# Kernel tuning notes

Measured on AMD Instinct MI355X. Metric: run time of the kernel, lower is better.

The kernel has to match this reference:

```python
import jax, jax.numpy as jnp
import numpy as np

N = 100000   # nodes
E = 800000   # edges
IN = 128     # input feature dim
H = 2        # heads
C = 64       # hidden_dim (per-head channels)
OUT = 40     # classes
L = 3        # num_layers
EPS = 1e-16  # matches torch_geometric.utils.softmax denominator eps


def setup_inputs() -> dict:
    key = jax.random.key(0)
    ks = jax.random.split(key, 4 * L + 6)
    inp = {}
    inp["x"] = jax.random.normal(ks[0], (N, IN), dtype=jnp.float32)
    inp["edge_index"] = jax.random.randint(ks[1], (2, E), 0, N, dtype=jnp.int32)
    dims = [IN] + [H * C] * (L - 1)
    ki = 2
    for l in range(L):
        d = dims[l]
        inp[f"W{l}"] = jax.random.normal(ks[ki], (H * C, d), dtype=jnp.float32) / np.float32(np.sqrt(d)); ki += 1
        inp[f"b{l}"] = jnp.zeros((H * C,), dtype=jnp.float32)
        inp[f"al{l}"] = jax.random.normal(ks[ki], (H, C), dtype=jnp.float32) * 0.1; ki += 1
        inp[f"ar{l}"] = jax.random.normal(ks[ki], (H, C), dtype=jnp.float32) * 0.1; ki += 1
    inp["Wp1"] = jax.random.normal(ks[ki], (C, H * C), dtype=jnp.float32) / np.float32(np.sqrt(H * C)); ki += 1
    inp["bp1"] = jnp.zeros((C,), dtype=jnp.float32)
    inp["Wp2"] = jax.random.normal(ks[ki], (OUT, C), dtype=jnp.float32) / np.float32(np.sqrt(C)); ki += 1
    inp["bp2"] = jnp.zeros((OUT,), dtype=jnp.float32)
    return inp


def _gat_layer(x, W, b, al, ar, src, dst):
    # lin_l == lin_r (shared weights in the original)
    h = (x @ W.T + b).reshape(-1, H, C)          # [N, H, C]
    alpha_l = al * h                              # source-side scores [N, H, C]
    alpha_r = ar * h                              # target-side scores [N, H, C]
    # per-edge raw attention logits; NOTE: original computes leaky_relu(alpha)
    # but then applies softmax to the RAW sum (faithful to source code).
    e = alpha_r[dst] + alpha_l[src]               # [E, H, C]
    m = jax.ops.segment_max(e, dst, num_segments=N)
    w = jnp.exp(e - m[dst])
    s = jax.ops.segment_sum(w, dst, num_segments=N)
    att = w / (s[dst] + EPS)                      # segment softmax per target node
    out = jax.ops.segment_sum(att * h[src], dst, num_segments=N)  # [N, H, C]
    return out.reshape(-1, H * C)


def reference(x, edge_index, W0, b0, al0, ar0, W1, b1, al1, ar1, W2, b2, al2, ar2,
              Wp1, bp1, Wp2, bp2):
    src, dst = edge_index[0], edge_index[1]
    layers = [(W0, b0, al0, ar0), (W1, b1, al1, ar1), (W2, b2, al2, ar2)]
    h = x
    for (W, b, al, ar) in layers:
        h = _gat_layer(h, W, b, al, ar, src, dst)
        h = jax.nn.relu(h)  # dropout p=0 -> identity
    h = h @ Wp1.T + bp1
    h = h @ Wp2.T + bp2
    return jax.nn.log_softmax(h, axis=1)
```

## Files before the change

kernel.cpp:

```cpp
#include <hip/hip_runtime.h>
#include <hip/hip_bf16.h>
#include <math.h>

#define NN 100000
#define EE 800000
#define DD 128
#define OUTC 40

typedef short bf16x8 __attribute__((ext_vector_type(8)));
typedef float f32x4 __attribute__((ext_vector_type(4)));

__device__ __forceinline__ ushort f2bf(float f) {
  unsigned u = __float_as_uint(f);
  u = (u + 0x7FFFu + ((u >> 16) & 1u)) >> 16;
  return (ushort)u;
}
__device__ __forceinline__ float bflo(unsigned u) { return __uint_as_float(u << 16); }
__device__ __forceinline__ float bfhi(unsigned u) { return __uint_as_float(u & 0xFFFF0000u); }

__device__ __forceinline__ int swz(int row, int kbyte) {
  return row * 256 + (kbyte ^ ((row & 7) << 4));
}

__global__ void k_hist(const int* __restrict__ dst, int* __restrict__ deg, int e) {
  int i = blockIdx.x * 256 + threadIdx.x;
  if (i < e) atomicAdd(&deg[dst[i]], 1);
}

__global__ __launch_bounds__(1024) void k_scan1(const int* __restrict__ deg, int* __restrict__ rp,
                                                int* __restrict__ bsum, int n) {
  __shared__ int s[1024];
  int t = threadIdx.x;
  int i = blockIdx.x * 1024 + t;
  s[t] = (i < n) ? deg[i] : 0;
  __syncthreads();
  for (int off = 1; off < 1024; off <<= 1) {
    int x = (t >= off) ? s[t - off] : 0;
    __syncthreads();
    s[t] += x;
    __syncthreads();
  }
  if (i < n) rp[i + 1] = s[t];
  if (t == 1023) bsum[blockIdx.x] = s[1023];
}

__global__ __launch_bounds__(128) void k_scan2(int* __restrict__ bsum, int nb) {
  __shared__ int s[128];
  int t = threadIdx.x;
  s[t] = (t < nb) ? bsum[t] : 0;
  __syncthreads();
  for (int off = 1; off < 128; off <<= 1) {
    int x = (t >= off) ? s[t - off] : 0;
    __syncthreads();
    s[t] += x;
    __syncthreads();
  }
  if (t < nb) bsum[t] = s[t];
}

__global__ void k_scan3(int* __restrict__ rp, const int* __restrict__ bsum,
                        int* __restrict__ cursor, int n) {
  int i = blockIdx.x * 256 + threadIdx.x;
  if (i == 0) { rp[0] = 0; cursor[0] = 0; }
  if (i < n) {
    int blk = i >> 10;
    int v = rp[i + 1] + ((blk > 0) ? bsum[blk - 1] : 0);
    rp[i + 1] = v;
    cursor[i + 1] = v;
  }
}

__global__ void k_scatter(const int* __restrict__ src, const int* __restrict__ dst,
                          int* __restrict__ cursor, int* __restrict__ col, int e) {
  int i = blockIdx.x * 256 + threadIdx.x;
  if (i < e) {
    int d = dst[i];
    int pos = atomicAdd(&cursor[d], 1);
    col[pos] = src[i];
  }
}

template<int NOUT, bool INF32, bool OUTBF>
__global__ __launch_bounds__(256, 2) void k_mfma_gemm(const void* __restrict__ xin,
                                                      const float* __restrict__ W,
                                                      const float* __restrict__ bias,
                                                      void* __restrict__ outp, int n) {
  __shared__ __align__(16) char lds[32768 + NOUT * 256];
  const int t = threadIdx.x;
  const int node0 = blockIdx.x * 128;

  if (INF32) {
#pragma unroll
    for (int p = 0; p < 16; ++p) {
      int F = p * 256 + t;
      int r = F >> 5, cchunk = F & 31;
      int node = node0 + r;
      float4 v = make_float4(0.f, 0.f, 0.f, 0.f);
      if (node < n) v = *(const float4*)((const float*)xin + (size_t)node * DD + cchunk * 4);
      ushort q[4] = {f2bf(v.x), f2bf(v.y), f2bf(v.z), f2bf(v.w)};
      *(unsigned long long*)(lds + swz(r, cchunk * 8)) = *(unsigned long long*)q;
    }
  } else {
#pragma unroll
    for (int p = 0; p < 8; ++p) {
      int F = p * 256 + t;
      int r = F >> 4, cchunk = F & 15;
      int node = node0 + r;
      uint4 v = make_uint4(0u, 0u, 0u, 0u);
      if (node < n) v = *(const uint4*)((const ushort*)xin + (size_t)node * DD + cchunk * 8);
      *(uint4*)(lds + swz(r, cchunk * 16)) = v;
    }
  }
  {
    constexpr int WPASS = NOUT / 8;
#pragma unroll
    for (int p = 0; p < WPASS; ++p) {
      int F = p * 256 + t;
      int r = F >> 5, cchunk = F & 31;
      float4 v = *(const float4*)(W + (size_t)r * DD + cchunk * 4);
      ushort q[4] = {f2bf(v.x), f2bf(v.y), f2bf(v.z), f2bf(v.w)};
      *(unsigned long long*)(lds + 32768 + swz(r, cchunk * 8)) = *(unsigned long long*)q;
    }
  }
  __syncthreads();

  const int lane = t & 63;
  const int l15 = lane & 15;
  const int lkb = (lane >> 4) * 16;
  const int wrow0 = (t >> 6) * 32;
  constexpr int NJ = NOUT / 16;

  f32x4 acc[2][NJ];
#pragma unroll
  for (int j = 0; j < NJ; ++j) {
    float bv = bias[j * 16 + l15];
    acc[0][j] = (f32x4){bv, bv, bv, bv};
    acc[1][j] = (f32x4){bv, bv, bv, bv};
  }

#pragma unroll
  for (int c = 0; c < 4; ++c) {
    bf16x8 a0 = *(const bf16x8*)(lds + swz(wrow0 + l15, c * 64 + lkb));
    bf16x8 a1 = *(const bf16x8*)(lds + swz(wrow0 + 16 + l15, c * 64 + lkb));
#pragma unroll
    for (int j = 0; j < NJ; ++j) {
      bf16x8 b = *(const bf16x8*)(lds + 32768 + swz(j * 16 + l15, c * 64 + lkb));
      acc[0][j] = __builtin_amdgcn_mfma_f32_16x16x32_bf16(a0, b, acc[0][j], 0, 0, 0);
      acc[1][j] = __builtin_amdgcn_mfma_f32_16x16x32_bf16(a1, b, acc[1][j], 0, 0, 0);
    }
  }

  const int rbase = wrow0 + (lane >> 4) * 4;
#pragma unroll
  for (int i = 0; i < 2; ++i) {
#pragma unroll
    for (int r = 0; r < 4; ++r) {
      int node = node0 + rbase + i * 16 + r;
      if (node < n) {
#pragma unroll
        for (int j = 0; j < NJ; ++j) {
          if (OUTBF)
            ((ushort*)outp)[(size_t)node * NOUT + j * 16 + l15] = f2bf(acc[i][j][r]);
          else
            ((float*)outp)[(size_t)node * NOUT + j * 16 + l15] = acc[i][j][r];
        }
      }
    }
  }
}

__global__ __launch_bounds__(256) void k_gat_agg(const ushort* __restrict__ h, const int* __restrict__ rp,
                                                 const int* __restrict__ col, const float* __restrict__ al,
                                                 const float* __restrict__ ar, ushort* __restrict__ out, int n) {
  int node = blockIdx.x * 4 + (threadIdx.x >> 6);
  int lane = threadIdx.x & 63;
  if (node >= n) return;
  const unsigned* hu = (const unsigned*)h;
  float al0 = al[2 * lane], al1 = al[2 * lane + 1];
  unsigned ud = hu[(unsigned)(node * 64 + lane)];
  float base0 = ar[2 * lane] * bflo(ud);
  float base1 = ar[2 * lane + 1] * bfhi(ud);
  int beg = __builtin_amdgcn_readfirstlane(rp[node]);
  int end = __builtin_amdgcn_readfirstlane(rp[node + 1]);
  float num0 = 0.f, num1 = 0.f, den0 = 0.f, den1 = 0.f;
#define ACCUM(U) { \
    float h0 = bflo(U), h1 = bfhi(U); \
    float w0 = __expf(fmaf(al0, h0, base0)); \
    float w1 = __expf(fmaf(al1, h1, base1)); \
    den0 += w0; den1 += w1; \
    num0 = fmaf(w0, h0, num0); num1 = fmaf(w1, h1, num1); }
  int j = beg;
  for (; j + 4 <= end; j += 4) {
    int s0 = __builtin_amdgcn_readfirstlane(col[j]);
    int s1 = __builtin_amdgcn_readfirstlane(col[j + 1]);
    int s2 = __builtin_amdgcn_readfirstlane(col[j + 2]);
    int s3 = __builtin_amdgcn_readfirstlane(col[j + 3]);
    unsigned u0 = hu[(unsigned)(s0 * 64 + lane)];
    unsigned u1 = hu[(unsigned)(s1 * 64 + lane)];
    unsigned u2 = hu[(unsigned)(s2 * 64 + lane)];
    unsigned u3 = hu[(unsigned)(s3 * 64 + lane)];
    ACCUM(u0); ACCUM(u1); ACCUM(u2); ACCUM(u3);
  }
  for (; j < end; ++j) {
    int s = __builtin_amdgcn_readfirstlane(col[j]);
    unsigned u = hu[(unsigned)(s * 64 + lane)];
    ACCUM(u);
  }
#undef ACCUM
  float o0 = fmaxf(num0 / (den0 + 1e-16f), 0.f);
  float o1 = fmaxf(num1 / (den1 + 1e-16f), 0.f);
  ((unsigned*)out)[(unsigned)(node * 64 + lane)] = (unsigned)f2bf(o0) | ((unsigned)f2bf(o1) << 16);
}

__global__ __launch_bounds__(256, 4) void k_fin2(const float* __restrict__ h1,
                                                 const float* __restrict__ Wp2,
                                                 const float* __restrict__ bp2,
                                                 float* __restrict__ out, int n) {
  int node = blockIdx.x * 256 + threadIdx.x;
  if (node >= n) return;
  float u[OUTC];
#pragma unroll
  for (int o = 0; o < OUTC; ++o) u[o] = bp2[o];
  const float* hp = h1 + (size_t)node * 64;
#pragma unroll
  for (int kc = 0; kc < 64; kc += 16) {
    float hv[16];
#pragma unroll
    for (int q = 0; q < 16; q += 4) *(float4*)&hv[q] = *(const float4*)&hp[kc + q];
#pragma unroll
    for (int o = 0; o < OUTC; ++o) {
      const float* wr = Wp2 + o * 64 + kc;
#pragma unroll
      for (int q = 0; q < 16; ++q) u[o] = fmaf(hv[q], wr[q], u[o]);
    }
  }
  float m = u[0];
#pragma unroll
  for (int o = 1; o < OUTC; ++o) m = fmaxf(m, u[o]);
  float ssum = 0.f;
#pragma unroll
  for (int o = 0; o < OUTC; ++o) ssum += __expf(u[o] - m);
  float ls = __logf(ssum) + m;
  float* op = out + (size_t)node * OUTC;
#pragma unroll
  for (int o = 0; o < OUTC; o += 4)
    *(float4*)&op[o] = make_float4(u[o] - ls, u[o + 1] - ls, u[o + 2] - ls, u[o + 3] - ls);
}

extern "C" void kernel_launch(void* const* d_in, const int* in_sizes, int n_in,
                              void* d_out, int out_size, void* d_ws, size_t ws_size,
                              hipStream_t stream) {
  const float* x   = (const float*)d_in[0];
  const int*   ei  = (const int*)d_in[1];
  const float* W[3]  = {(const float*)d_in[2],  (const float*)d_in[6],  (const float*)d_in[10]};
  const float* B[3]  = {(const float*)d_in[3],  (const float*)d_in[7],  (const float*)d_in[11]};
  const float* AL[3] = {(const float*)d_in[4],  (const float*)d_in[8],  (const float*)d_in[12]};
  const float* AR[3] = {(const float*)d_in[5],  (const float*)d_in[9],  (const float*)d_in[13]};
  const float* Wp1 = (const float*)d_in[14];
  const float* bp1 = (const float*)d_in[15];
  const float* Wp2 = (const float*)d_in[16];
  const float* bp2 = (const float*)d_in[17];
  float* outp = (float*)d_out;

  const int n = NN, e = EE;
  const int* srcp = ei;
  const int* dstp = ei + e;

  char* ws = (char*)d_ws;
  size_t off = 0;
  auto alloc = [&](size_t bytes) { void* p = ws + off; off = (off + bytes + 255) & ~(size_t)255; return p; };
  ushort* bhA = (ushort*)alloc((size_t)n * DD * 2);
  ushort* bhB = (ushort*)alloc((size_t)n * DD * 2);
  float*  h1f = (float*)alloc((size_t)n * 64 * 4);
  int*   deg   = (int*)alloc((size_t)n * 4);
  int*   rp    = (int*)alloc((size_t)(n + 1) * 4);
  int*   cursor= (int*)alloc((size_t)(n + 1) * 4);
  int*   bsum  = (int*)alloc(1024 * 4);
  int*   col   = (int*)alloc((size_t)e * 4);
  (void)ws_size;

  hipMemsetAsync(deg, 0, (size_t)n * 4, stream);
  k_hist<<<(e + 255) / 256, 256, 0, stream>>>(dstp, deg, e);
  int nb = (n + 1023) / 1024;
  k_scan1<<<nb, 1024, 0, stream>>>(deg, rp, bsum, n);
  k_scan2<<<1, 128, 0, stream>>>(bsum, nb);
  k_scan3<<<(n + 255) / 256, 256, 0, stream>>>(rp, bsum, cursor, n);
  k_scatter<<<(e + 255) / 256, 256, 0, stream>>>(srcp, dstp, cursor, col, e);

  const int gblocks = (n + 127) / 128;
  const int ablocks = (n + 3) / 4;
  k_mfma_gemm<128, true, true><<<gblocks, 256, 0, stream>>>(x, W[0], B[0], bhA, n);
  k_gat_agg<<<ablocks, 256, 0, stream>>>(bhA, rp, col, AL[0], AR[0], bhB, n);
  for (int l = 1; l < 3; ++l) {
    k_mfma_gemm<128, false, true><<<gblocks, 256, 0, stream>>>(bhB, W[l], B[l], bhA, n);
    k_gat_agg<<<ablocks, 256, 0, stream>>>(bhA, rp, col, AL[l], AR[l], bhB, n);
  }
  k_mfma_gemm<64, false, false><<<gblocks, 256, 0, stream>>>(bhB, Wp1, bp1, h1f, n);
  k_fin2<<<(n + 255) / 256, 256, 0, stream>>>(h1f, Wp2, bp2, outp, n);
}
```

Before: 431.9 us.

## Fuse final projection GEMM with classifier and log-softmax; unroll aggregation by eight

Merges the Wp1 MFMA GEMM and the Wp2 classifier plus log_softmax into one kernel. The 64-wide fp32 intermediate is staged in LDS instead of written to and read back from global memory, and one launch is dropped. The GAT aggregation loop gains an 8-way unrolled gather stage and a 2-way tail, putting more neighbor loads in flight. The catch is that only half the threads do the classifier phase, and the larger LDS use may cut occupancy.

```diff
diff --git a/kernel.cpp b/kernel.cpp
--- a/kernel.cpp
+++ b/kernel.cpp
@@ -80,12 +80,12 @@
   }
 }
 
-template<int NOUT, bool INF32, bool OUTBF>
+template<bool INF32>
 __global__ __launch_bounds__(256, 2) void k_mfma_gemm(const void* __restrict__ xin,
                                                       const float* __restrict__ W,
                                                       const float* __restrict__ bias,
-                                                      void* __restrict__ outp, int n) {
-  __shared__ __align__(16) char lds[32768 + NOUT * 256];
+                                                      ushort* __restrict__ outp, int n) {
+  __shared__ __align__(16) char lds[65536];
   const int t = threadIdx.x;
   const int node0 = blockIdx.x * 128;
 
@@ -112,9 +112,8 @@
     }
   }
   {
-    constexpr int WPASS = NOUT / 8;
-#pragma unroll
-    for (int p = 0; p < WPASS; ++p) {
+#pragma unroll
+    for (int p = 0; p < 16; ++p) {
       int F = p * 256 + t;
       int r = F >> 5, cchunk = F & 31;
       float4 v = *(const float4*)(W + (size_t)r * DD + cchunk * 4);
@@ -128,11 +127,10 @@
   const int l15 = lane & 15;
   const int lkb = (lane >> 4) * 16;
   const int wrow0 = (t >> 6) * 32;
-  constexpr int NJ = NOUT / 16;
-
-  f32x4 acc[2][NJ];
-#pragma unroll
-  for (int j = 0; j < NJ; ++j) {
+
+  f32x4 acc[2][8];
+#pragma unroll
+  for (int j = 0; j < 8; ++j) {
     float bv = bias[j * 16 + l15];
     acc[0][j] = (f32x4){bv, bv, bv, bv};
     acc[1][j] = (f32x4){bv, bv, bv, bv};
@@ -143,7 +141,7 @@
     bf16x8 a0 = *(const bf16x8*)(lds + swz(wrow0 + l15, c * 64 + lkb));
     bf16x8 a1 = *(const bf16x8*)(lds + swz(wrow0 + 16 + l15, c * 64 + lkb));
 #pragma unroll
-    for (int j = 0; j < NJ; ++j) {
+    for (int j = 0; j < 8; ++j) {
       bf16x8 b = *(const bf16x8*)(lds + 32768 + swz(j * 16 + l15, c * 64 + lkb));
       acc[0][j] = __builtin_amdgcn_mfma_f32_16x16x32_bf16(a0, b, acc[0][j], 0, 0, 0);
       acc[1][j] = __builtin_amdgcn_mfma_f32_16x16x32_bf16(a1, b, acc[1][j], 0, 0, 0);
@@ -158,12 +156,8 @@
       int node = node0 + rbase + i * 16 + r;
       if (node < n) {
 #pragma unroll
-        for (int j = 0; j < NJ; ++j) {
-          if (OUTBF)
-            ((ushort*)outp)[(size_t)node * NOUT + j * 16 + l15] = f2bf(acc[i][j][r]);
-          else
-            ((float*)outp)[(size_t)node * NOUT + j * 16 + l15] = acc[i][j][r];
-        }
+        for (int j = 0; j < 8; ++j)
+          outp[(size_t)node * DD + j * 16 + l15] = f2bf(acc[i][j][r]);
       }
     }
   }
@@ -190,6 +184,26 @@
     den0 += w0; den1 += w1; \
     num0 = fmaf(w0, h0, num0); num1 = fmaf(w1, h1, num1); }
   int j = beg;
+  for (; j + 8 <= end; j += 8) {
+    int s0 = __builtin_amdgcn_readfirstlane(col[j]);
+    int s1 = __builtin_amdgcn_readfirstlane(col[j + 1]);
+    int s2 = __builtin_amdgcn_readfirstlane(col[j + 2]);
+    int s3 = __builtin_amdgcn_readfirstlane(col[j + 3]);
+    int s4 = __builtin_amdgcn_readfirstlane(col[j + 4]);
+    int s5 = __builtin_amdgcn_readfirstlane(col[j + 5]);
+    int s6 = __builtin_amdgcn_readfirstlane(col[j + 6]);
+    int s7 = __builtin_amdgcn_readfirstlane(col[j + 7]);
+    unsigned u0 = hu[(unsigned)(s0 * 64 + lane)];
+    unsigned u1 = hu[(unsigned)(s1 * 64 + lane)];
+    unsigned u2 = hu[(unsigned)(s2 * 64 + lane)];
+    unsigned u3 = hu[(unsigned)(s3 * 64 + lane)];
+    unsigned u4 = hu[(unsigned)(s4 * 64 + lane)];
+    unsigned u5 = hu[(unsigned)(s5 * 64 + lane)];
+    unsigned u6 = hu[(unsigned)(s6 * 64 + lane)];
+    unsigned u7 = hu[(unsigned)(s7 * 64 + lane)];
+    ACCUM(u0); ACCUM(u1); ACCUM(u2); ACCUM(u3);
+    ACCUM(u4); ACCUM(u5); ACCUM(u6); ACCUM(u7);
+  }
   for (; j + 4 <= end; j += 4) {
     int s0 = __builtin_amdgcn_readfirstlane(col[j]);
     int s1 = __builtin_amdgcn_readfirstlane(col[j + 1]);
@@ -201,6 +215,13 @@
     unsigned u3 = hu[(unsigned)(s3 * 64 + lane)];
     ACCUM(u0); ACCUM(u1); ACCUM(u2); ACCUM(u3);
   }
+  for (; j + 2 <= end; j += 2) {
+    int s0 = __builtin_amdgcn_readfirstlane(col[j]);
+    int s1 = __builtin_amdgcn_readfirstlane(col[j + 1]);
+    unsigned u0 = hu[(unsigned)(s0 * 64 + lane)];
+    unsigned u1 = hu[(unsigned)(s1 * 64 + lane)];
+    ACCUM(u0); ACCUM(u1);
+  }
   for (; j < end; ++j) {
     int s = __builtin_amdgcn_readfirstlane(col[j]);
     unsigned u = hu[(unsigned)(s * 64 + lane)];
@@ -212,39 +233,108 @@
   ((unsigned*)out)[(unsigned)(node * 64 + lane)] = (unsigned)f2bf(o0) | ((unsigned)f2bf(o1) << 16);
 }
 
-__global__ __launch_bounds__(256, 4) void k_fin2(const float* __restrict__ h1,
-                                                 const float* __restrict__ Wp2,
-                                                 const float* __restrict__ bp2,
-                                                 float* __restrict__ out, int n) {
-  int node = blockIdx.x * 256 + threadIdx.x;
-  if (node >= n) return;
-  float u[OUTC];
-#pragma unroll
-  for (int o = 0; o < OUTC; ++o) u[o] = bp2[o];
-  const float* hp = h1 + (size_t)node * 64;
-#pragma unroll
-  for (int kc = 0; kc < 64; kc += 16) {
-    float hv[16];
-#pragma unroll
-    for (int q = 0; q < 16; q += 4) *(float4*)&hv[q] = *(const float4*)&hp[kc + q];
-#pragma unroll
-    for (int o = 0; o < OUTC; ++o) {
-      const float* wr = Wp2 + o * 64 + kc;
-#pragma unroll
-      for (int q = 0; q < 16; ++q) u[o] = fmaf(hv[q], wr[q], u[o]);
-    }
-  }
-  float m = u[0];
-#pragma unroll
-  for (int o = 1; o < OUTC; ++o) m = fmaxf(m, u[o]);
-  float ssum = 0.f;
-#pragma unroll
-  for (int o = 0; o < OUTC; ++o) ssum += __expf(u[o] - m);
-  float ls = __logf(ssum) + m;
-  float* op = out + (size_t)node * OUTC;
-#pragma unroll
-  for (int o = 0; o < OUTC; o += 4)
-    *(float4*)&op[o] = make_float4(u[o] - ls, u[o + 1] - ls, u[o + 2] - ls, u[o + 3] - ls);
+__global__ __launch_bounds__(256, 2) void k_final_fused(const ushort* __restrict__ xin,
+                                                        const float* __restrict__ W1,
+                                                        const float* __restrict__ b1,
+                                                        const float* __restrict__ Wp2,
+                                                        const float* __restrict__ bp2,
+                                                        float* __restrict__ out, int n) {
+  __shared__ __align__(16) char lds[49152];
+  const int t = threadIdx.x;
+  const int node0 = blockIdx.x * 128;
+
+#pragma unroll
+  for (int p = 0; p < 8; ++p) {
+    int F = p * 256 + t;
+    int r = F >> 4, cchunk = F & 15;
+    int node = node0 + r;
+    uint4 v = make_uint4(0u, 0u, 0u, 0u);
+    if (node < n) v = *(const uint4*)(xin + (size_t)node * DD + cchunk * 8);
+    *(uint4*)(lds + swz(r, cchunk * 16)) = v;
+  }
+#pragma unroll
+  for (int p = 0; p < 8; ++p) {
+    int F = p * 256 + t;
+    int r = F >> 5, cchunk = F & 31;
+    float4 v = *(const float4*)(W1 + (size_t)r * DD + cchunk * 4);
+    ushort q[4] = {f2bf(v.x), f2bf(v.y), f2bf(v.z), f2bf(v.w)};
+    *(unsigned long long*)(lds + 32768 + swz(r, cchunk * 8)) = *(unsigned long long*)q;
+  }
+  __syncthreads();
+
+  const int lane = t & 63;
+  const int l15 = lane & 15;
+  const int lkb = (lane >> 4) * 16;
+  const int wrow0 = (t >> 6) * 32;
+
+  f32x4 acc[2][4];
+#pragma unroll
+  for (int j = 0; j < 4; ++j) {
+    float bv = b1[j * 16 + l15];
+    acc[0][j] = (f32x4){bv, bv, bv, bv};
+    acc[1][j] = (f32x4){bv, bv, bv, bv};
+  }
+#pragma unroll
+  for (int c = 0; c < 4; ++c) {
+    bf16x8 a0 = *(const bf16x8*)(lds + swz(wrow0 + l15, c * 64 + lkb));
+    bf16x8 a1 = *(const bf16x8*)(lds + swz(wrow0 + 16 + l15, c * 64 + lkb));
+#pragma unroll
+    for (int j = 0; j < 4; ++j) {
+      bf16x8 b = *(const bf16x8*)(lds + 32768 + swz(j * 16 + l15, c * 64 + lkb));
+      acc[0][j] = __builtin_amdgcn_mfma_f32_16x16x32_bf16(a0, b, acc[0][j], 0, 0, 0);
+      acc[1][j] = __builtin_amdgcn_mfma_f32_16x16x32_bf16(a1, b, acc[1][j], 0, 0, 0);
+    }
+  }
+  __syncthreads();
+
+  float* h1L = (float*)lds;
+  float* wpL = (float*)(lds + 34816);
+  const int rbase = wrow0 + (lane >> 4) * 4;
+#pragma unroll
+  for (int i = 0; i < 2; ++i)
+#pragma unroll
+    for (int r = 0; r < 4; ++r) {
+      int row = rbase + i * 16 + r;
+#pragma unroll
+      for (int j = 0; j < 4; ++j)
+        h1L[row * 68 + j * 16 + l15] = acc[i][j][r];
+    }
+#pragma unroll
+  for (int p = 0; p < 10; ++p) {
+    int f = p * 256 + t;
+    int o = f >> 6, q = f & 63;
+    wpL[o * 68 + q] = Wp2[f];
+  }
+  __syncthreads();
+
+  if (t < 128) {
+    int node = node0 + t;
+    if (node < n) {
+      float u[OUTC];
+#pragma unroll
+      for (int o = 0; o < OUTC; ++o) u[o] = bp2[o];
+#pragma unroll
+      for (int qc = 0; qc < 16; ++qc) {
+        f32x4 hv = *(const f32x4*)&h1L[t * 68 + qc * 4];
+#pragma unroll
+        for (int o = 0; o < OUTC; ++o) {
+          f32x4 w = *(const f32x4*)&wpL[o * 68 + qc * 4];
+          u[o] = fmaf(hv[3], w[3], fmaf(hv[2], w[2], fmaf(hv[1], w[1], fmaf(hv[0], w[0], u[o]))));
+        }
+      }
+      float m = u[0];
+#pragma unroll
+      for (int o = 1; o < OUTC; ++o) m = fmaxf(m, u[o]);
+      float ssum = 0.f;
+#pragma unroll
+      for (int o = 0; o < OUTC; ++o) ssum += __expf(u[o] - m);
+      float ls = __logf(ssum) + m;
+      float* op = out + (size_t)node * OUTC;
+#pragma unroll
+      for (int o = 0; o < OUTC; o += 4)
+        *(float4*)&op[o] = make_float4(u[o] - ls, u[o + 1] - ls, u[o + 2] - ls, u[o + 3] - ls);
+    }
+  }
 }
 
 extern "C" void kernel_launch(void* const* d_in, const int* in_sizes, int n_in,
@@ -271,7 +361,6 @@
   auto alloc = [&](size_t bytes) { void* p = ws + off; off = (off + bytes + 255) & ~(size_t)255; return p; };
   ushort* bhA = (ushort*)alloc((size_t)n * DD * 2);
   ushort* bhB = (ushort*)alloc((size_t)n * DD * 2);
-  float*  h1f = (float*)alloc((size_t)n * 64 * 4);
   int*   deg   = (int*)alloc((size_t)n * 4);
   int*   rp    = (int*)alloc((size_t)(n + 1) * 4);
   int*   cursor= (int*)alloc((size_t)(n + 1) * 4);
@@ -289,12 +378,11 @@
 
   const int gblocks = (n + 127) / 128;
   const int ablocks = (n + 3) / 4;
-  k_mfma_gemm<128, true, true><<<gblocks, 256, 0, stream>>>(x, W[0], B[0], bhA, n);
+  k_mfma_gemm<true><<<gblocks, 256, 0, stream>>>(x, W[0], B[0], bhA, n);
   k_gat_agg<<<ablocks, 256, 0, stream>>>(bhA, rp, col, AL[0], AR[0], bhB, n);
   for (int l = 1; l < 3; ++l) {
-    k_mfma_gemm<128, false, true><<<gblocks, 256, 0, stream>>>(bhB, W[l], B[l], bhA, n);
+    k_mfma_gemm<false><<<gblocks, 256, 0, stream>>>(bhB, W[l], B[l], bhA, n);
     k_gat_agg<<<ablocks, 256, 0, stream>>>(bhA, rp, col, AL[l], AR[l], bhB, n);
   }
-  k_mfma_gemm<64, false, false><<<gblocks, 256, 0, stream>>>(bhB, Wp1, bp1, h1f, n);
-  k_fin2<<<(n + 255) / 256, 256, 0, stream>>>(h1f, Wp2, bp2, outp, n);
-}
+  k_final_fused<<<gblocks, 256, 0, stream>>>(bhB, Wp1, bp1, Wp2, bp2, outp, n);
+}
```

After: 413.6 us. 1.04x faster.
